# Optimization experiments

Hardware: AMD Instinct MI355X
Metric: run time of the kernel (lower is better)

Reference implementation:

```python
import jax, jax.numpy as jnp
import numpy as np

N_NODES = 50000
N_EDGES = 1600000
IN_DIM = 128
OUT_DIM = 64
NEG_SLOPE = 0.2


def setup_inputs() -> dict:
    key = jax.random.key(0)
    k1, k2, k3, k4, k5, k6 = jax.random.split(key, 6)
    in_feat = jax.random.normal(k1, (N_NODES, IN_DIM), dtype=jnp.float32)
    edge_list = jax.random.randint(k2, (2, N_EDGES), 0, N_NODES, dtype=jnp.int64)
    # GATConv params (heads=1): linear weight (no bias), att_src, att_dst, out bias
    W = jax.random.normal(k3, (IN_DIM, OUT_DIM), dtype=jnp.float32) / np.sqrt(IN_DIM)
    a_src = jax.random.normal(k4, (OUT_DIM,), dtype=jnp.float32) / np.sqrt(OUT_DIM)
    a_dst = jax.random.normal(k5, (OUT_DIM,), dtype=jnp.float32) / np.sqrt(OUT_DIM)
    bias = jax.random.normal(k6, (OUT_DIM,), dtype=jnp.float32) * 0.01
    return {"in_feat": in_feat, "edge_list": edge_list, "W": W,
            "a_src": a_src, "a_dst": a_dst, "bias": bias}


def reference(in_feat, edge_list, W, a_src, a_dst, bias):
    # Linear transform: [N, F_in] -> [N, F_out]
    x = in_feat @ W
    src, dst = edge_list[0], edge_list[1]
    # Per-node attention halves, gathered per edge
    alpha_src = x @ a_src  # [N]
    alpha_dst = x @ a_dst  # [N]
    e = alpha_src[src] + alpha_dst[dst]                      # [E]
    e = jnp.where(e > 0, e, NEG_SLOPE * e)                   # leaky_relu
    # Segment softmax over destination node
    e_max = jax.ops.segment_max(e, dst, num_segments=N_NODES)  # [N]
    e_exp = jnp.exp(e - e_max[dst])                          # [E]
    denom = jax.ops.segment_sum(e_exp, dst, num_segments=N_NODES)  # [N]
    alpha = e_exp / (denom[dst] + 1e-16)                     # [E]
    # Weighted scatter-add of source messages into destinations
    msg = x[src] * alpha[:, None]                            # [E, F_out]
    out = jax.ops.segment_sum(msg, dst, num_segments=N_NODES)  # [N, F_out]
    return out + bias
```

## Files before the change

### kernel.cpp

```cpp
#include <hip/hip_runtime.h>
#include <hip/hip_fp16.h>
#include <math.h>

#define IN_DIM 128
#define OUT_DIM 64
#define NEG_SLOPE 0.2f
#define PART_CH 12288
#define PART_RPT 24
#define PBINS 400
#define PBUCK_CAP 5120
#define BUCK_NODES 32
#define BUCK_CAP 1536

typedef __attribute__((ext_vector_type(8))) short bf16x8;
typedef __attribute__((ext_vector_type(4))) float f32x4;

__device__ inline unsigned bf16u(float f) {
    unsigned u = __float_as_uint(f);
    return (u + 0x7fffu + ((u >> 16) & 1u)) >> 16;
}

__device__ inline bf16x8 ldfrag(const ushort* p) {
    union { uint2 u2[2]; bf16x8 v; } u;
    u.u2[0] = *(const uint2*)p;
    u.u2[1] = *(const uint2*)(p + 16);
    return u.v;
}

__global__ __launch_bounds__(256) void k_gemm(
        const float* __restrict__ feat, const float* __restrict__ W,
        const float* __restrict__ a_src, const float* __restrict__ a_dst,
        ushort* __restrict__ xb, float* __restrict__ asrc,
        float* __restrict__ adst, int* __restrict__ gcur, int N) {
    __shared__ ushort fA[64][136];
    __shared__ ushort wB[64][136];
    int t = threadIdx.x;
    int row0 = blockIdx.x << 6;

    if (blockIdx.x == 0) {
        gcur[t] = 0;
        gcur[t + 256] = 0;
    }

    {
        const float4* Wv = (const float4*)W;
#pragma unroll
        for (int j = 0; j < 8; ++j) {
            int i = t + 256 * j;
            float4 wv = Wv[i];
            int k = i >> 4, c0 = (i & 15) << 2;
            wB[c0 + 0][k] = (ushort)bf16u(wv.x);
            wB[c0 + 1][k] = (ushort)bf16u(wv.y);
            wB[c0 + 2][k] = (ushort)bf16u(wv.z);
            wB[c0 + 3][k] = (ushort)bf16u(wv.w);
        }
    }
    {
        int nrow = N - row0; if (nrow > 64) nrow = 64;
        int nv = nrow << 5;
        const float4* fv = (const float4*)(feat + (size_t)row0 * IN_DIM);
#pragma unroll
        for (int j = 0; j < 8; ++j) {
            int i = t + 256 * j;
            int row = i >> 5, k0 = (i & 31) << 2;
            ushort4 b;
            if (i < nv) {
                float4 f = fv[i];
                b = make_ushort4((ushort)bf16u(f.x), (ushort)bf16u(f.y),
                                 (ushort)bf16u(f.z), (ushort)bf16u(f.w));
            } else {
                b = make_ushort4(0, 0, 0, 0);
            }
            *(ushort4*)&fA[row][k0] = b;
        }
    }
    __syncthreads();

    int lane = t & 63, w = t >> 6;
    int col16 = lane & 15, kg = lane >> 4;
    int ar = (w << 4) + col16;
    f32x4 zero = {0.f, 0.f, 0.f, 0.f};
    f32x4 acc[4] = {zero, zero, zero, zero};

#pragma unroll
    for (int ks = 0; ks < 4; ++ks) {
        int K0 = (ks << 5) + (kg << 2);
        bf16x8 a = ldfrag(&fA[ar][K0]);
#pragma unroll
        for (int ct = 0; ct < 4; ++ct) {
            bf16x8 b = ldfrag(&wB[(ct << 4) + col16][K0]);
            acc[ct] = __builtin_amdgcn_mfma_f32_16x16x32_bf16(a, b, acc[ct], 0, 0, 0);
        }
    }

    float as[4], ad[4];
#pragma unroll
    for (int ct = 0; ct < 4; ++ct) {
        as[ct] = a_src[(ct << 4) + col16];
        ad[ct] = a_dst[(ct << 4) + col16];
    }
#pragma unroll
    for (int reg = 0; reg < 4; ++reg) {
        int row = row0 + (w << 4) + (kg << 2) + reg;
        float ps = acc[0][reg] * as[0] + acc[1][reg] * as[1] +
                   acc[2][reg] * as[2] + acc[3][reg] * as[3];
        float pd = acc[0][reg] * ad[0] + acc[1][reg] * ad[1] +
                   acc[2][reg] * ad[2] + acc[3][reg] * ad[3];
#pragma unroll
        for (int off = 1; off < 16; off <<= 1) {
            ps += __shfl_xor(ps, off);
            pd += __shfl_xor(pd, off);
        }
        if (row < N) {
            ushort* xp = xb + ((size_t)row << 6) + col16;
            xp[0]  = (ushort)bf16u(acc[0][reg]);
            xp[16] = (ushort)bf16u(acc[1][reg]);
            xp[32] = (ushort)bf16u(acc[2][reg]);
            xp[48] = (ushort)bf16u(acc[3][reg]);
            if (col16 == 0) { asrc[row] = ps; adst[row] = pd; }
        }
    }
}

__global__ __launch_bounds__(512) void k_part(const int* __restrict__ el,
                                              int* __restrict__ gcur,
                                              unsigned* __restrict__ grecs,
                                              int E) {
    __shared__ unsigned srt[PART_CH];
    __shared__ int hist[PBINS], nbeg[PBINS], lbase[PBINS];
    __shared__ int wsum[8];
    int t = threadIdx.x;
    int start = blockIdx.x * PART_CH;
    int len = E - start < PART_CH ? E - start : PART_CH;
    const int* srcp = el + start;
    const int* dstp = el + E + start;

    for (int i = t; i < PBINS; i += 512) hist[i] = 0;
    __syncthreads();

    int dreg[PART_RPT], rreg[PART_RPT];
#pragma unroll
    for (int j = 0; j < PART_RPT; ++j) {
        int i = t + 512 * j;
        if (i < len) {
            int d = dstp[i];
            dreg[j] = d;
            rreg[j] = atomicAdd(&hist[d >> 7], 1);
        }
    }
    __syncthreads();

    int lane = t & 63, wv = t >> 6;
    int c = t < PBINS ? hist[t] : 0;
    int inc = c;
#pragma unroll
    for (int off = 1; off < 64; off <<= 1) {
        int n = __shfl_up(inc, off);
        if (lane >= off) inc += n;
    }
    if (lane == 63) wsum[wv] = inc;
    __syncthreads();
    int woff = 0;
#pragma unroll
    for (int i = 0; i < 8; ++i) woff += (i < wv) ? wsum[i] : 0;
    if (t < PBINS) {
        int excl = woff + inc - c;
        nbeg[t] = excl;
        if (c) lbase[t] = atomicAdd(&gcur[t], c);
    }
    __syncthreads();

#pragma unroll
    for (int j = 0; j < PART_RPT; ++j) {
        int i = t + 512 * j;
        if (i < len) {
            int sx = srcp[i];
            int d = dreg[j];
            srt[nbeg[d >> 7] + rreg[j]] = (unsigned)sx | ((unsigned)d << 16);
        }
    }
    __syncthreads();

    for (int i = t; i < len; i += 512) {
        unsigned r = srt[i];
        int bn = r >> 23;
        int slot = lbase[bn] + (i - nbeg[bn]);
        if (slot < PBUCK_CAP) grecs[(size_t)bn * PBUCK_CAP + slot] = r;
    }
}

__global__ __launch_bounds__(256) void k_bg(
        const unsigned* __restrict__ grecs, const int* __restrict__ gcur,
        const float* __restrict__ asrc, const float* __restrict__ adst,
        const ushort* __restrict__ xb, const float* __restrict__ bias,
        float* __restrict__ out, int N) {
    __shared__ unsigned srt[BUCK_CAP];
    __shared__ int ncnt[BUCK_NODES], nbeg[BUCK_NODES], ncur[BUCK_NODES];
    __shared__ float adst_l[BUCK_NODES];
    int t = threadIdx.x;
    int b = blockIdx.x;
    int parent = b >> 2, q = b & 3;
    int node0 = b << 5;
    int cnt = gcur[parent];
    if (cnt > PBUCK_CAP) cnt = PBUCK_CAP;
    const unsigned* rbase = grecs + (size_t)parent * PBUCK_CAP;

    if (t < BUCK_NODES) {
        ncnt[t] = 0;
        int node = node0 + t;
        adst_l[t] = node < N ? adst[node] : 0.f;
    }
    __syncthreads();
    for (int i = t; i < cnt; i += 256) {
        int loc = (rbase[i] >> 16) & 127;
        if ((loc >> 5) == q) atomicAdd(&ncnt[loc & 31], 1);
    }
    __syncthreads();
    if (t < 64) {
        int v = t < BUCK_NODES ? ncnt[t] : 0;
        int inc = v;
#pragma unroll
        for (int off = 1; off < BUCK_NODES; off <<= 1) {
            int n = __shfl_up(inc, off);
            if (t >= off) inc += n;
        }
        if (t < BUCK_NODES) {
            int excl = inc - v;
            nbeg[t] = excl;
            ncur[t] = excl;
        }
    }
    __syncthreads();
    for (int i = t; i < cnt; i += 256) {
        unsigned r = rbase[i];
        int loc = (r >> 16) & 127;
        if ((loc >> 5) == q) {
            int s = r & 0xFFFF;
            float e = asrc[s] + adst_l[loc & 31];
            e = e > 0.f ? e : NEG_SLOPE * e;
            float p = __expf(e);
            int slot = atomicAdd(&ncur[loc & 31], 1);
            srt[slot] = (unsigned)s |
                        ((unsigned)__half_as_ushort(__float2half(p)) << 16);
        }
    }
    __syncthreads();

    int g = t >> 3, sl = t & 7;
    int node = node0 + g;
    if (node >= N) return;
    const ushort* xsl = xb + (sl << 3);
    int c0 = sl << 3;
    float4 ba = *(const float4*)(bias + c0);
    float4 bb = *(const float4*)(bias + c0 + 4);
    int b0 = nbeg[g], b1 = b0 + ncnt[g];
    float acc[8] = {0.f, 0.f, 0.f, 0.f, 0.f, 0.f, 0.f, 0.f};
    float denom = 0.f;
#pragma unroll 4
    for (int i = b0; i < b1; ++i) {
        unsigned r = srt[i];
        float p = __half2float(__ushort_as_half((unsigned short)(r >> 16)));
        uint4 xv = *(const uint4*)(xsl + ((size_t)(r & 0xFFFF) << 6));
        denom += p;
        acc[0] += p * __uint_as_float(xv.x << 16);
        acc[1] += p * __uint_as_float(xv.x & 0xffff0000u);
        acc[2] += p * __uint_as_float(xv.y << 16);
        acc[3] += p * __uint_as_float(xv.y & 0xffff0000u);
        acc[4] += p * __uint_as_float(xv.z << 16);
        acc[5] += p * __uint_as_float(xv.z & 0xffff0000u);
        acc[6] += p * __uint_as_float(xv.w << 16);
        acc[7] += p * __uint_as_float(xv.w & 0xffff0000u);
    }
    float inv = 1.f / (denom + 1e-16f);
    float4 o0 = make_float4(acc[0] * inv + ba.x, acc[1] * inv + ba.y,
                            acc[2] * inv + ba.z, acc[3] * inv + ba.w);
    float4 o1 = make_float4(acc[4] * inv + bb.x, acc[5] * inv + bb.y,
                            acc[6] * inv + bb.z, acc[7] * inv + bb.w);
    float* orow = out + ((size_t)node << 6) + c0;
    *(float4*)orow = o0;
    *(float4*)(orow + 4) = o1;
}

extern "C" void kernel_launch(void* const* d_in, const int* in_sizes, int n_in,
                              void* d_out, int out_size, void* d_ws, size_t ws_size,
                              hipStream_t stream) {
    const float* feat  = (const float*)d_in[0];
    const int*   el    = (const int*)d_in[1];
    const float* W     = (const float*)d_in[2];
    const float* a_src = (const float*)d_in[3];
    const float* a_dst = (const float*)d_in[4];
    const float* bias  = (const float*)d_in[5];
    float* out = (float*)d_out;

    const int N = in_sizes[0] / IN_DIM;
    const int E = in_sizes[1] / 2;
    const int NPB = (E + PART_CH - 1) / PART_CH;
    const int NPAR = (N + 127) >> 7;
    const int NBUCK = (N + BUCK_NODES - 1) / BUCK_NODES;

    char* ws = (char*)d_ws;
    ushort* xb      = (ushort*)ws;   ws += (size_t)N * OUT_DIM * 2;
    float* asrc     = (float*)ws;    ws += (size_t)N * 4;
    float* adst     = (float*)ws;    ws += (size_t)N * 4;
    int*   gcur     = (int*)ws;      ws += 512 * 4;
    unsigned* grecs = (unsigned*)ws; ws += (size_t)NPAR * PBUCK_CAP * 4;

    k_gemm<<<(N + 63) / 64, 256, 0, stream>>>(feat, W, a_src, a_dst, xb, asrc,
                                              adst, gcur, N);
    k_part<<<NPB, 512, 0, stream>>>(el, gcur, grecs, E);
    k_bg<<<NBUCK, 256, 0, stream>>>(grecs, gcur, asrc, adst, xb, bias, out, N);
}
```

Baseline: 69.86 us.

## Replace global-atomic bucket scatter with per-block sorted runs and offset table

The partition kernel no longer reserves slots in global parent buckets with atomics. Each block now writes its locally sorted chunk contiguously and records per-bin start offsets in a table. The bucket kernel gathers its parent bin's records from every partition block's run into a shared queue, and chunk size is halved to get more partition blocks. This removes global atomics and scattered writes, and drops the gcur zeroing in the GEMM kernel. In exchange, each bucket block must read an offset table row per partition block (around 261 runs) and issue many small, partially filled wavefront loads.

```diff
diff --git a/kernel.cpp b/kernel.cpp
--- a/kernel.cpp
+++ b/kernel.cpp
@@ -5,10 +5,10 @@
 #define IN_DIM 128
 #define OUT_DIM 64
 #define NEG_SLOPE 0.2f
-#define PART_CH 12288
-#define PART_RPT 24
-#define PBINS 400
-#define PBUCK_CAP 5120
+#define PART_CH 6144
+#define PART_RPT 12
+#define PBINS 391
+#define OBSTRIDE 392
 #define BUCK_NODES 32
 #define BUCK_CAP 1536
 
@@ -31,16 +31,11 @@
         const float* __restrict__ feat, const float* __restrict__ W,
         const float* __restrict__ a_src, const float* __restrict__ a_dst,
         ushort* __restrict__ xb, float* __restrict__ asrc,
-        float* __restrict__ adst, int* __restrict__ gcur, int N) {
+        float* __restrict__ adst, int N) {
     __shared__ ushort fA[64][136];
     __shared__ ushort wB[64][136];
     int t = threadIdx.x;
     int row0 = blockIdx.x << 6;
-
-    if (blockIdx.x == 0) {
-        gcur[t] = 0;
-        gcur[t + 256] = 0;
-    }
 
     {
         const float4* Wv = (const float4*)W;
@@ -123,11 +118,11 @@
 }
 
 __global__ __launch_bounds__(512) void k_part(const int* __restrict__ el,
-                                              int* __restrict__ gcur,
                                               unsigned* __restrict__ grecs,
+                                              int* __restrict__ obeg,
                                               int E) {
     __shared__ unsigned srt[PART_CH];
-    __shared__ int hist[PBINS], nbeg[PBINS], lbase[PBINS];
+    __shared__ int hist[PBINS], nbeg[PBINS];
     __shared__ int wsum[8];
     int t = threadIdx.x;
     int start = blockIdx.x * PART_CH;
@@ -163,11 +158,9 @@
     int woff = 0;
 #pragma unroll
     for (int i = 0; i < 8; ++i) woff += (i < wv) ? wsum[i] : 0;
-    if (t < PBINS) {
-        int excl = woff + inc - c;
-        nbeg[t] = excl;
-        if (c) lbase[t] = atomicAdd(&gcur[t], c);
-    }
+    if (t < PBINS) nbeg[t] = woff + inc - c;
+    if (t < PBINS) obeg[blockIdx.x * OBSTRIDE + t] = start + woff + inc - c;
+    if (t == PBINS) obeg[blockIdx.x * OBSTRIDE + PBINS] = start + len;
     __syncthreads();
 
 #pragma unroll
@@ -181,39 +174,53 @@
     }
     __syncthreads();
 
-    for (int i = t; i < len; i += 512) {
-        unsigned r = srt[i];
-        int bn = r >> 23;
-        int slot = lbase[bn] + (i - nbeg[bn]);
-        if (slot < PBUCK_CAP) grecs[(size_t)bn * PBUCK_CAP + slot] = r;
-    }
+    for (int i = t; i < len; i += 512) grecs[start + i] = srt[i];
 }
 
 __global__ __launch_bounds__(256) void k_bg(
-        const unsigned* __restrict__ grecs, const int* __restrict__ gcur,
+        const unsigned* __restrict__ grecs, const int* __restrict__ obeg,
         const float* __restrict__ asrc, const float* __restrict__ adst,
         const ushort* __restrict__ xb, const float* __restrict__ bias,
-        float* __restrict__ out, int N) {
+        float* __restrict__ out, int N, int npb) {
+    __shared__ int rb[264], re[264];
+    __shared__ unsigned rawq[BUCK_CAP];
     __shared__ unsigned srt[BUCK_CAP];
     __shared__ int ncnt[BUCK_NODES], nbeg[BUCK_NODES], ncur[BUCK_NODES];
     __shared__ float adst_l[BUCK_NODES];
+    __shared__ int qn;
     int t = threadIdx.x;
     int b = blockIdx.x;
     int parent = b >> 2, q = b & 3;
     int node0 = b << 5;
-    int cnt = gcur[parent];
-    if (cnt > PBUCK_CAP) cnt = PBUCK_CAP;
-    const unsigned* rbase = grecs + (size_t)parent * PBUCK_CAP;
 
     if (t < BUCK_NODES) {
         ncnt[t] = 0;
         int node = node0 + t;
         adst_l[t] = node < N ? adst[node] : 0.f;
     }
-    __syncthreads();
-    for (int i = t; i < cnt; i += 256) {
-        int loc = (rbase[i] >> 16) & 127;
-        if ((loc >> 5) == q) atomicAdd(&ncnt[loc & 31], 1);
+    if (t == 0) qn = 0;
+    for (int i = t; i < npb; i += 256) {
+        rb[i] = obeg[i * OBSTRIDE + parent];
+        re[i] = obeg[i * OBSTRIDE + parent + 1];
+    }
+    __syncthreads();
+
+    int w = t >> 6, lane = t & 63;
+    for (int r = w; r < npb; r += 4) {
+        int beg = rb[r], n = re[r] - beg;
+        for (int off = 0; off < n; off += 64) {
+            unsigned rec = 0;
+            int ok = 0;
+            if (off + lane < n) {
+                rec = grecs[beg + off + lane];
+                ok = (((rec >> 16) & 127) >> 5) == (unsigned)q;
+            }
+            if (ok) {
+                int pos = atomicAdd(&qn, 1);
+                atomicAdd(&ncnt[(rec >> 16) & 31], 1);
+                if (pos < BUCK_CAP) rawq[pos] = rec;
+            }
+        }
     }
     __syncthreads();
     if (t < 64) {
@@ -231,18 +238,18 @@
         }
     }
     __syncthreads();
-    for (int i = t; i < cnt; i += 256) {
-        unsigned r = rbase[i];
-        int loc = (r >> 16) & 127;
-        if ((loc >> 5) == q) {
-            int s = r & 0xFFFF;
-            float e = asrc[s] + adst_l[loc & 31];
-            e = e > 0.f ? e : NEG_SLOPE * e;
-            float p = __expf(e);
-            int slot = atomicAdd(&ncur[loc & 31], 1);
+    int qcnt = qn < BUCK_CAP ? qn : BUCK_CAP;
+    for (int i = t; i < qcnt; i += 256) {
+        unsigned rec = rawq[i];
+        int loc5 = (rec >> 16) & 31;
+        int s = rec & 0xFFFF;
+        float e = asrc[s] + adst_l[loc5];
+        e = e > 0.f ? e : NEG_SLOPE * e;
+        float p = __expf(e);
+        int slot = atomicAdd(&ncur[loc5], 1);
+        if (slot < BUCK_CAP)
             srt[slot] = (unsigned)s |
                         ((unsigned)__half_as_ushort(__float2half(p)) << 16);
-        }
     }
     __syncthreads();
 
@@ -254,6 +261,7 @@
     float4 ba = *(const float4*)(bias + c0);
     float4 bb = *(const float4*)(bias + c0 + 4);
     int b0 = nbeg[g], b1 = b0 + ncnt[g];
+    if (b1 > BUCK_CAP) b1 = BUCK_CAP;
     float acc[8] = {0.f, 0.f, 0.f, 0.f, 0.f, 0.f, 0.f, 0.f};
     float denom = 0.f;
 #pragma unroll 4
@@ -295,18 +303,17 @@
     const int N = in_sizes[0] / IN_DIM;
     const int E = in_sizes[1] / 2;
     const int NPB = (E + PART_CH - 1) / PART_CH;
-    const int NPAR = (N + 127) >> 7;
     const int NBUCK = (N + BUCK_NODES - 1) / BUCK_NODES;
 
     char* ws = (char*)d_ws;
     ushort* xb      = (ushort*)ws;   ws += (size_t)N * OUT_DIM * 2;
     float* asrc     = (float*)ws;    ws += (size_t)N * 4;
     float* adst     = (float*)ws;    ws += (size_t)N * 4;
-    int*   gcur     = (int*)ws;      ws += 512 * 4;
-    unsigned* grecs = (unsigned*)ws; ws += (size_t)NPAR * PBUCK_CAP * 4;
+    unsigned* grecs = (unsigned*)ws; ws += (size_t)NPB * PART_CH * 4;
+    int* obeg       = (int*)ws;      ws += (size_t)NPB * OBSTRIDE * 4;
 
     k_gemm<<<(N + 63) / 64, 256, 0, stream>>>(feat, W, a_src, a_dst, xb, asrc,
-                                              adst, gcur, N);
-    k_part<<<NPB, 512, 0, stream>>>(el, gcur, grecs, E);
-    k_bg<<<NBUCK, 256, 0, stream>>>(grecs, gcur, asrc, adst, xb, bias, out, N);
-}
+                                              adst, N);
+    k_part<<<NPB, 512, 0, stream>>>(el, grecs, obeg, E);
+    k_bg<<<NBUCK, 256, 0, stream>>>(grecs, obeg, asrc, adst, xb, bias, out, N, NPB);
+}
```

Measured after the change: 87.92 us. 1.26x slower.
